# Performance work log

Measured on AMD Instinct MI355X. Metric: run time of the kernel, lower is better.

Reference implementation:

```python
import jax, jax.numpy as jnp
import numpy as np

VOCAB = 50000
WORD_DIM = 300
HIDDEN = 300
REL = 3
B = 512        # batch of (premise, hypothesis) tree pairs
LEAVES = 256   # leaves per complete binary tree (depth 8)


def setup_inputs() -> dict:
    key = jax.random.key(0)
    ks = jax.random.split(key, 6)
    sc = lambda k, shape, s: jax.random.normal(k, shape, dtype=jnp.float32) * s
    return {
        "word_ids": jax.random.randint(ks[0], (B, 2, LEAVES), 0, VOCAB),
        "embedding": sc(ks[1], (VOCAB, WORD_DIM), 0.1),
        "W_leaf": sc(ks[2], (HIDDEN, WORD_DIM), 0.05),   # word2hidden (no bias)
        "W_h": sc(ks[3], (HIDDEN, 2 * HIDDEN), 0.05),    # hidden2hidden
        "b_h": jnp.zeros((HIDDEN,), jnp.float32),
        "W_cls": sc(ks[4], (REL, 2 * HIDDEN), 0.05),
        "b_cls": jnp.zeros((REL,), jnp.float32),
    }


def _encode_trees(word_ids, embedding, W_leaf, W_h, b_h):
    # word_ids: [B, 2, L] leaf token ids of complete binary trees.
    # Leaf: h = word2hidden(embedding(id))  (no bias, no activation)
    h = embedding[word_ids] @ W_leaf.T                     # [B, 2, L, H]
    # Postorder combine, level-synchronous: parent = hidden2hidden(cat(l, r))
    n = h.shape[2]
    while n > 1:
        left = h[:, :, 0::2, :]
        right = h[:, :, 1::2, :]
        h = jnp.concatenate([left, right], axis=-1) @ W_h.T + b_h
        n //= 2
    return h[:, :, 0, :]                                   # [B, 2, H] roots


def reference(word_ids, embedding, W_leaf, W_h, b_h, W_cls, b_cls):
    roots = _encode_trees(word_ids, embedding, W_leaf, W_h, b_h)  # [B, 2, H]
    feat = jax.nn.sigmoid(roots.reshape(roots.shape[0], -1))      # cat(p, h) -> [B, 2H]
    logits = feat @ W_cls.T + b_cls                               # [B, REL]
    return jax.nn.log_softmax(logits, axis=-1)
```

## Files before the change

kernel.cpp:

```cpp
#include <hip/hip_runtime.h>
#include <hip/hip_bf16.h>

typedef __hip_bfloat16 bf16;
typedef __attribute__((ext_vector_type(8))) short short8;
typedef __attribute__((ext_vector_type(4))) float float4v;
typedef __attribute__((ext_vector_type(4))) short short4v;

__device__ __forceinline__ short f2bs(float x) {
    bf16 b = __float2bfloat16(x);
    return *reinterpret_cast<short*>(&b);
}
__device__ __forceinline__ float bs2f(short s) {
    bf16 b = *reinterpret_cast<bf16*>(&s);
    return __bfloat162float(b);
}

#define GLL16(g, l) __builtin_amdgcn_global_load_lds(                      \
    (const __attribute__((address_space(1))) void*)(g),                    \
    (__attribute__((address_space(3))) void*)(l), 16, 0, 0)


__global__ __launch_bounds__(256) void conv_emb(
    const float* __restrict__ src, short* __restrict__ dst)
{
    const int idx = blockIdx.x * 256 + threadIdx.x;
    if (idx >= 50176 * 80) return;
    const int row = idx / 80;
    const int k4  = (idx - row * 80) * 4;
    short4v v = (short4v)0;
    if (row < 50000 && k4 < 300) {
        const float4v f = *reinterpret_cast<const float4v*>(
            src + (long)row * 300 + k4);
#pragma unroll
        for (int j = 0; j < 4; ++j) v[j] = f2bs(f[j]);
    }
    *(short4v*)&dst[(long)row * 320 + k4] = v;
}

__global__ __launch_bounds__(256) void conv_w(
    const float* __restrict__ W_h, const float* __restrict__ W_leaf,
    const float* __restrict__ b_h, short* __restrict__ Bh,
    short* __restrict__ Bleaf, float* __restrict__ biasp)
{
    const int idx = blockIdx.x * 256 + threadIdx.x;
    if (idx < 204800) {
        const int row = idx / 640, k = idx - row * 640;
        float v = 0.f;
        if (row < 300) {
            if (k < 300)                  v = W_h[row * 600 + k];
            else if (k >= 320 && k < 620) v = W_h[row * 600 + k - 20];
        }
        Bh[idx] = f2bs(v);
    } else if (idx < 307200) {
        const int i = idx - 204800;
        const int row = i / 320, k = i - row * 320;
        Bleaf[i] = (row < 300 && k < 300) ? f2bs(W_leaf[row * 300 + k])
                                          : (short)0;
    } else if (idx < 307520) {
        const int i = idx - 307200;
        biasp[i] = (i < 300) ? b_h[i] : 0.f;
    }
}

template <int KE, int GMODE, bool BIAS>
__global__ __launch_bounds__(256, 2) void mfma_gemm(
    const short* __restrict__ Xsrc, const int* __restrict__ wid,
    const short* __restrict__ emb, const short* __restrict__ Wp,
    const float* __restrict__ biasp, short* __restrict__ out)
{
    static_assert(GMODE != 2 || KE == 640, "pair-gather requires KE=640");
    __shared__ __align__(16) short As[2][128 * 32];
    __shared__ __align__(16) short Bs[2][320 * 32];

    const int tid  = threadIdx.x;
    const int lane = tid & 63;
    const int w    = tid >> 6;
    const int wm   = w >> 1, wn = w & 1;
    const long m0  = (long)blockIdx.x * 128;

    const int s_q   = lane & 3;
    const int r_off = lane >> 2;

    const char* gL[2];
    const char* gR[2];
#pragma unroll
    for (int j = 0; j < 2; ++j) {
        const int r = (w * 2 + j) * 16 + r_off;
        const int q = s_q ^ ((r >> 1) & 3);
        if (GMODE == 2) {
            const long node = m0 + r;
            gL[j] = (const char*)emb + (long)wid[2 * node]     * 640 + q * 16;
            gR[j] = (const char*)emb + (long)wid[2 * node + 1] * 640 + q * 16;
        } else {
            gL[j] = (const char*)Xsrc + (m0 + r) * (long)(KE * 2) + q * 16;
            gR[j] = gL[j];
        }
    }
    const char* gB[5];
#pragma unroll
    for (int j = 0; j < 5; ++j) {
        const int r = (w * 5 + j) * 16 + r_off;
        const int q = s_q ^ ((r >> 1) & 3);
        gB[j] = (const char*)Wp + r * (long)(KE * 2) + q * 16;
    }

    int oA[4];
#pragma unroll
    for (int t = 0; t < 4; ++t) {
        const int row = wm * 64 + t * 16 + (lane & 15);
        const int s   = (lane >> 4) ^ ((row >> 1) & 3);
        oA[t] = row * 32 + s * 8;
    }
    int oB[10];
#pragma unroll
    for (int u = 0; u < 10; ++u) {
        const int n = wn * 160 + u * 16 + (lane & 15);
        const int s = (lane >> 4) ^ ((n >> 1) & 3);
        oB[u] = n * 32 + s * 8;
    }

    auto stage = [&](int buf, int kc) {
        char* baseA = (char*)&As[buf][0];
        char* baseB = (char*)&Bs[buf][0];
        if (GMODE == 2) {
            const bool lft = (kc < 10);
            const int off = (lft ? kc : kc - 10) * 64;
            GLL16((lft ? gL[0] : gR[0]) + off, baseA + (w * 2 + 0) * 1024);
            GLL16((lft ? gL[1] : gR[1]) + off, baseA + (w * 2 + 1) * 1024);
        } else {
            const int off = kc * 64;
            GLL16(gL[0] + off, baseA + (w * 2 + 0) * 1024);
            GLL16(gL[1] + off, baseA + (w * 2 + 1) * 1024);
        }
        const int offb = kc * 64;
#pragma unroll
        for (int j = 0; j < 5; ++j)
            GLL16(gB[j] + offb, baseB + (w * 5 + j) * 1024);
    };

    float4v acc[4][10];
#pragma unroll
    for (int t = 0; t < 4; ++t)
#pragma unroll
        for (int u = 0; u < 10; ++u) acc[t][u] = (float4v)0.f;

    const int NCH = KE / 32;
    stage(0, 0);
    for (int kc = 0; kc < NCH; ++kc) {
        const int cur = kc & 1;
        if (kc + 1 < NCH) {
            stage(cur ^ 1, kc + 1);
            asm volatile("s_waitcnt vmcnt(7)" ::: "memory");
        } else {
            asm volatile("s_waitcnt vmcnt(0)" ::: "memory");
        }
        __builtin_amdgcn_s_barrier();
        __builtin_amdgcn_sched_barrier(0);

        const short* bA = &As[cur][0];
        const short* bB = &Bs[cur][0];
        short8 a[4], b[10];
#pragma unroll
        for (int t = 0; t < 4; ++t) a[t] = *(const short8*)(bA + oA[t]);
#pragma unroll
        for (int u = 0; u < 10; ++u) b[u] = *(const short8*)(bB + oB[u]);
#pragma unroll
        for (int u = 0; u < 10; ++u)
#pragma unroll
            for (int t = 0; t < 4; ++t)
                acc[t][u] = __builtin_amdgcn_mfma_f32_16x16x32_bf16(
                    a[t], b[u], acc[t][u], 0, 0, 0);
        __builtin_amdgcn_s_barrier();
    }

#pragma unroll
    for (int u = 0; u < 10; ++u) {
        const int c = wn * 160 + u * 16 + (lane & 15);
        const float bv = BIAS ? biasp[c] : 0.f;
#pragma unroll
        for (int t = 0; t < 4; ++t) {
            const long mb = m0 + wm * 64 + t * 16 + (lane >> 4) * 4;
#pragma unroll
            for (int r4 = 0; r4 < 4; ++r4)
                out[(mb + r4) * 320 + c] = f2bs(acc[t][u][r4] + bv);
        }
    }
}

template<int MA, bool STREAM, bool TOROOTS>
__device__ __forceinline__ void tree_level(
    const int w, const int lane,
    const short* Ain, short* Aout, short* Bs, short* Astage,
    const char* gA, const char* gB0, const char* gB1, const char* gB2,
    const char* gB3, const char* gB4, const float* __restrict__ biasp)
{
    constexpr int MT  = (MA + 15) / 16;
    constexpr int TPW = MT * 5;
    const int lrow = lane & 15;
    const int hi   = lane >> 4;

    float4v acc[TPW];
#pragma unroll
    for (int t = 0; t < TPW; ++t) acc[t] = (float4v)0.f;

    for (int kc = 0; kc < 20; ++kc) {
        GLL16(gB0 + kc * 64, (char*)Bs + (w * 5 + 0) * 1024);
        GLL16(gB1 + kc * 64, (char*)Bs + (w * 5 + 1) * 1024);
        GLL16(gB2 + kc * 64, (char*)Bs + (w * 5 + 2) * 1024);
        GLL16(gB3 + kc * 64, (char*)Bs + (w * 5 + 3) * 1024);
        GLL16(gB4 + kc * 64, (char*)Bs + (w * 5 + 4) * 1024);
        if (STREAM)
            GLL16(gA + (kc >= 10 ? 640 : 0) + (kc % 10) * 64,
                  (char*)Astage + w * 1024);
        asm volatile("s_waitcnt vmcnt(0)" ::: "memory");
        __builtin_amdgcn_s_barrier();
        __builtin_amdgcn_sched_barrier(0);

#pragma unroll
        for (int t = 0; t < TPW; ++t) {
            const int g  = w + t * 4;
            const int mt = g / 20, nt = g % 20;
            int row = mt * 16 + lrow;
            if (MA < 16) row = (lrow < MA) ? lrow : 0;
            const int sa = hi ^ ((row >> 1) & 3);
            const short* pa = STREAM
                ? (Astage + row * 32 + sa * 8)
                : (Ain + kc * (MA * 32) + row * 32 + sa * 8);
            const int n  = nt * 16 + lrow;
            const int sb = hi ^ ((n >> 1) & 3);
            const short8 a = *(const short8*)pa;
            const short8 b = *(const short8*)(Bs + n * 32 + sb * 8);
            acc[t] = __builtin_amdgcn_mfma_f32_16x16x32_bf16(
                a, b, acc[t], 0, 0, 0);
        }
        __builtin_amdgcn_s_barrier();
    }

#pragma unroll
    for (int t = 0; t < TPW; ++t) {
        const int g  = w + t * 4;
        const int mt = g / 20, nt = g % 20;
        const int c  = nt * 16 + lrow;
        const float bv = biasp[c];
#pragma unroll
        for (int r4 = 0; r4 < 4; ++r4) {
            const int mb = mt * 16 + hi * 4 + r4;
            if (mb < MA) {
                const short v = f2bs(acc[t][r4] + bv);
                if (TOROOTS) {
                    Aout[mb * 320 + c] = v;
                } else {
                    constexpr int MN = MA / 2;
                    const int p  = (mb & 1) * 10 + (c >> 5);
                    const int m2 = mb >> 1;
                    const int q  = (c >> 3) & 3;
                    Aout[p * (MN * 32) + m2 * 32 +
                         (q ^ ((m2 >> 1) & 3)) * 8 + (c & 7)] = v;
                }
            }
        }
    }
    __syncthreads();
}

__global__ __launch_bounds__(256, 2) void subtree(
    const short* __restrict__ L2in, const short* __restrict__ Wp,
    const float* __restrict__ biasp, const float* __restrict__ W_cls,
    const float* __restrict__ b_cls, float* __restrict__ outp)
{
    __shared__ __align__(16) short Bs[320 * 32];
    __shared__ __align__(16) short AX[20 * 32 * 32];
    __shared__ __align__(16) short AY[10240];

    const int tid  = threadIdx.x;
    const int lane = tid & 63;
    const int w    = tid >> 6;
    const int s_q   = lane & 3;
    const int r_off = lane >> 2;
    const long base = (long)blockIdx.x * 128;

    const char* gB[5];
#pragma unroll
    for (int j = 0; j < 5; ++j) {
        const int r = (w * 5 + j) * 16 + r_off;
        const int q = s_q ^ ((r >> 1) & 3);
        gB[j] = (const char*)Wp + r * 1280L + q * 16;
    }
    const int rS = w * 16 + r_off;
    const int qS = s_q ^ ((rS >> 1) & 3);
    const char* gA3 = (const char*)L2in + (base + 2 * rS) * 640 + qS * 16;

    tree_level<64, true,  false>(w, lane, nullptr, AX, Bs, AY, gA3,
                                 gB[0], gB[1], gB[2], gB[3], gB[4], biasp);
    tree_level<32, false, false>(w, lane, AX, AY, Bs, nullptr, nullptr,
                                 gB[0], gB[1], gB[2], gB[3], gB[4], biasp);
    tree_level<16, false, false>(w, lane, AY, AX, Bs, nullptr, nullptr,
                                 gB[0], gB[1], gB[2], gB[3], gB[4], biasp);
    tree_level<8,  false, false>(w, lane, AX, AY, Bs, nullptr, nullptr,
                                 gB[0], gB[1], gB[2], gB[3], gB[4], biasp);
    tree_level<4,  false, false>(w, lane, AY, AX, Bs, nullptr, nullptr,
                                 gB[0], gB[1], gB[2], gB[3], gB[4], biasp);
    tree_level<2,  false, true >(w, lane, AX, AY, Bs, nullptr, nullptr,
                                 gB[0], gB[1], gB[2], gB[3], gB[4], biasp);

    if (w == 0) {
        float a0 = 0.f, a1 = 0.f, a2 = 0.f;
#pragma unroll
        for (int i = 0; i < 10; ++i) {
            const int k = lane + 64 * i;
            if (k < 600) {
                const int col = (k < 300) ? k : (320 + k - 300);
                const float f = 1.f / (1.f + __expf(-bs2f(AY[col])));
                a0 += f * W_cls[k];
                a1 += f * W_cls[600 + k];
                a2 += f * W_cls[1200 + k];
            }
        }
#pragma unroll
        for (int off = 32; off > 0; off >>= 1) {
            a0 += __shfl_down(a0, off);
            a1 += __shfl_down(a1, off);
            a2 += __shfl_down(a2, off);
        }
        if (lane == 0) {
            const int b = blockIdx.x;
            const float l0 = a0 + b_cls[0];
            const float l1 = a1 + b_cls[1];
            const float l2 = a2 + b_cls[2];
            const float m  = fmaxf(l0, fmaxf(l1, l2));
            const float s  = __expf(l0 - m) + __expf(l1 - m) + __expf(l2 - m);
            const float ls = m + __logf(s);
            outp[b * 3 + 0] = l0 - ls;
            outp[b * 3 + 1] = l1 - ls;
            outp[b * 3 + 2] = l2 - ls;
        }
    }
}

extern "C" void kernel_launch(void* const* d_in, const int* in_sizes, int n_in,
                              void* d_out, int out_size, void* d_ws, size_t ws_size,
                              hipStream_t stream)
{
    const int*   wid    = (const int*)d_in[0];
    const float* emb    = (const float*)d_in[1];
    const float* W_leaf = (const float*)d_in[2];
    const float* W_h    = (const float*)d_in[3];
    const float* b_h    = (const float*)d_in[4];
    const float* W_cls  = (const float*)d_in[5];
    const float* b_cls  = (const float*)d_in[6];
    float* outp = (float*)d_out;

    (void)in_sizes; (void)n_in; (void)out_size; (void)ws_size;

    char* ws = (char*)d_ws;
    short* bufA   = (short*)(ws);
    short* bufB   = (short*)(ws + 83886080);
    short* emb_bf = (short*)(ws + 83886080);
    short* Hv     = (short*)(ws + 125829120);
    short* Bleaf  = (short*)(ws + 157941760);
    short* Bh     = (short*)(ws + 158146560);
    float* biasp  = (float*)(ws + 158556160);

    conv_emb<<<(50176 * 80) / 256, 256, 0, stream>>>(emb, emb_bf);
    conv_w  <<<(307520 + 255) / 256, 256, 0, stream>>>(
        W_h, W_leaf, b_h, Bh, Bleaf, biasp);

    mfma_gemm<320, 0, false><<<50176 / 128, 256, 0, stream>>>(
        emb_bf, nullptr, nullptr, Bleaf, biasp, Hv);

    mfma_gemm<640, 2, true><<<131072 / 128, 256, 0, stream>>>(
        nullptr, wid, Hv, Bh, biasp, bufA);

    mfma_gemm<640, 0, true><<<65536 / 128, 256, 0, stream>>>(
        bufA, nullptr, nullptr, Bh, biasp, bufB);

    subtree<<<512, 256, 0, stream>>>(bufB, Bh, biasp, W_cls, b_cls, outp);
}
```

Baseline: 343.8 us.

## Process two trees per subtree block sharing weight tiles, merge conversion kernels

The subtree kernel now runs 512 threads handling two tree pairs per block. Waves 0-3 load the shared W_h tile into LDS while waves 4-7 stream both trees' level inputs, so each weight chunk is fetched once per two trees and the blocks are halved. The two fp32-to-bf16 conversion kernels are merged into one launch to save launch overhead. The costs are more LDS per block, occupancy capped at one 512-thread block, and load work concentrated on fewer waves.

```diff
diff --git a/kernel.cpp b/kernel.cpp
--- a/kernel.cpp
+++ b/kernel.cpp
@@ -19,45 +19,42 @@
     (const __attribute__((address_space(1))) void*)(g),                    \
     (__attribute__((address_space(3))) void*)(l), 16, 0, 0)
 
-
-__global__ __launch_bounds__(256) void conv_emb(
-    const float* __restrict__ src, short* __restrict__ dst)
+__global__ __launch_bounds__(256) void conv_all(
+    const float* __restrict__ emb, const float* __restrict__ W_h,
+    const float* __restrict__ W_leaf, const float* __restrict__ b_h,
+    short* __restrict__ emb_bf, short* __restrict__ Bh,
+    short* __restrict__ Bleaf, float* __restrict__ biasp)
 {
     const int idx = blockIdx.x * 256 + threadIdx.x;
-    if (idx >= 50176 * 80) return;
-    const int row = idx / 80;
-    const int k4  = (idx - row * 80) * 4;
-    short4v v = (short4v)0;
-    if (row < 50000 && k4 < 300) {
-        const float4v f = *reinterpret_cast<const float4v*>(
-            src + (long)row * 300 + k4);
-#pragma unroll
-        for (int j = 0; j < 4; ++j) v[j] = f2bs(f[j]);
-    }
-    *(short4v*)&dst[(long)row * 320 + k4] = v;
-}
-
-__global__ __launch_bounds__(256) void conv_w(
-    const float* __restrict__ W_h, const float* __restrict__ W_leaf,
-    const float* __restrict__ b_h, short* __restrict__ Bh,
-    short* __restrict__ Bleaf, float* __restrict__ biasp)
-{
-    const int idx = blockIdx.x * 256 + threadIdx.x;
-    if (idx < 204800) {
-        const int row = idx / 640, k = idx - row * 640;
+    if (idx < 4014080) {
+        const int row = idx / 80;
+        const int k4  = (idx - row * 80) * 4;
+        short4v v = (short4v)0;
+        if (row < 50000 && k4 < 300) {
+            const float4v f = *reinterpret_cast<const float4v*>(
+                emb + (long)row * 300 + k4);
+#pragma unroll
+            for (int j = 0; j < 4; ++j) v[j] = f2bs(f[j]);
+        }
+        *(short4v*)&emb_bf[(long)row * 320 + k4] = v;
+        return;
+    }
+    const int j = idx - 4014080;
+    if (j < 204800) {
+        const int row = j / 640, k = j - row * 640;
         float v = 0.f;
         if (row < 300) {
             if (k < 300)                  v = W_h[row * 600 + k];
             else if (k >= 320 && k < 620) v = W_h[row * 600 + k - 20];
         }
-        Bh[idx] = f2bs(v);
-    } else if (idx < 307200) {
-        const int i = idx - 204800;
+        Bh[j] = f2bs(v);
+    } else if (j < 307200) {
+        const int i = j - 204800;
         const int row = i / 320, k = i - row * 320;
         Bleaf[i] = (row < 300 && k < 300) ? f2bs(W_leaf[row * 300 + k])
                                           : (short)0;
-    } else if (idx < 307520) {
-        const int i = idx - 307200;
+    } else if (j < 307520) {
+        const int i = j - 307200;
         biasp[i] = (i < 300) ? b_h[i] : 0.f;
     }
 }
@@ -189,9 +186,11 @@
 
 template<int MA, bool STREAM, bool TOROOTS>
 __device__ __forceinline__ void tree_level(
-    const int w, const int lane,
-    const short* Ain, short* Aout, short* Bs, short* Astage,
-    const char* gA, const char* gB0, const char* gB1, const char* gB2,
+    const int w, const int wl, const int lane,
+    const short* Ain, short* Aout, short* Bs,
+    const short* myAst, short* Ast0, short* Ast1,
+    const char* gA0, const char* gA1,
+    const char* gB0, const char* gB1, const char* gB2,
     const char* gB3, const char* gB4, const float* __restrict__ biasp)
 {
     constexpr int MT  = (MA + 15) / 16;
@@ -204,27 +203,30 @@
     for (int t = 0; t < TPW; ++t) acc[t] = (float4v)0.f;
 
     for (int kc = 0; kc < 20; ++kc) {
-        GLL16(gB0 + kc * 64, (char*)Bs + (w * 5 + 0) * 1024);
-        GLL16(gB1 + kc * 64, (char*)Bs + (w * 5 + 1) * 1024);
-        GLL16(gB2 + kc * 64, (char*)Bs + (w * 5 + 2) * 1024);
-        GLL16(gB3 + kc * 64, (char*)Bs + (w * 5 + 3) * 1024);
-        GLL16(gB4 + kc * 64, (char*)Bs + (w * 5 + 4) * 1024);
-        if (STREAM)
-            GLL16(gA + (kc >= 10 ? 640 : 0) + (kc % 10) * 64,
-                  (char*)Astage + w * 1024);
+        if (w < 4) {
+            GLL16(gB0 + kc * 64, (char*)Bs + (w * 5 + 0) * 1024);
+            GLL16(gB1 + kc * 64, (char*)Bs + (w * 5 + 1) * 1024);
+            GLL16(gB2 + kc * 64, (char*)Bs + (w * 5 + 2) * 1024);
+            GLL16(gB3 + kc * 64, (char*)Bs + (w * 5 + 3) * 1024);
+            GLL16(gB4 + kc * 64, (char*)Bs + (w * 5 + 4) * 1024);
+        } else if (STREAM) {
+            const int off = (kc >= 10 ? 640 : 0) + (kc % 10) * 64;
+            GLL16(gA0 + off, (char*)Ast0 + (w - 4) * 1024);
+            GLL16(gA1 + off, (char*)Ast1 + (w - 4) * 1024);
+        }
         asm volatile("s_waitcnt vmcnt(0)" ::: "memory");
         __builtin_amdgcn_s_barrier();
         __builtin_amdgcn_sched_barrier(0);
 
 #pragma unroll
         for (int t = 0; t < TPW; ++t) {
-            const int g  = w + t * 4;
+            const int g  = wl + t * 4;
             const int mt = g / 20, nt = g % 20;
             int row = mt * 16 + lrow;
             if (MA < 16) row = (lrow < MA) ? lrow : 0;
             const int sa = hi ^ ((row >> 1) & 3);
             const short* pa = STREAM
-                ? (Astage + row * 32 + sa * 8)
+                ? (myAst + row * 32 + sa * 8)
                 : (Ain + kc * (MA * 32) + row * 32 + sa * 8);
             const int n  = nt * 16 + lrow;
             const int sb = hi ^ ((n >> 1) & 3);
@@ -238,7 +240,7 @@
 
 #pragma unroll
     for (int t = 0; t < TPW; ++t) {
-        const int g  = w + t * 4;
+        const int g  = wl + t * 4;
         const int mt = g / 20, nt = g % 20;
         const int c  = nt * 16 + lrow;
         const float bv = biasp[c];
@@ -263,54 +265,69 @@
     __syncthreads();
 }
 
-__global__ __launch_bounds__(256, 2) void subtree(
+__global__ __launch_bounds__(512, 1) void subtree(
     const short* __restrict__ L2in, const short* __restrict__ Wp,
     const float* __restrict__ biasp, const float* __restrict__ W_cls,
     const float* __restrict__ b_cls, float* __restrict__ outp)
 {
     __shared__ __align__(16) short Bs[320 * 32];
-    __shared__ __align__(16) short AX[20 * 32 * 32];
-    __shared__ __align__(16) short AY[10240];
+    __shared__ __align__(16) short AXs[2][20 * 32 * 32];
+    __shared__ __align__(16) short AYs[2][10240];
+    __shared__ __align__(16) short Ast[2][2048];
 
     const int tid  = threadIdx.x;
     const int lane = tid & 63;
     const int w    = tid >> 6;
+    const int wl   = w & 3;
+    const int grp  = w >> 2;
     const int s_q   = lane & 3;
     const int r_off = lane >> 2;
-    const long base = (long)blockIdx.x * 128;
 
     const char* gB[5];
 #pragma unroll
     for (int j = 0; j < 5; ++j) {
-        const int r = (w * 5 + j) * 16 + r_off;
+        const int r = (wl * 5 + j) * 16 + r_off;
         const int q = s_q ^ ((r >> 1) & 3);
         gB[j] = (const char*)Wp + r * 1280L + q * 16;
     }
-    const int rS = w * 16 + r_off;
+    const int wa = (w >= 4) ? (w - 4) : 0;
+    const int rS = wa * 16 + r_off;
     const int qS = s_q ^ ((rS >> 1) & 3);
-    const char* gA3 = (const char*)L2in + (base + 2 * rS) * 640 + qS * 16;
-
-    tree_level<64, true,  false>(w, lane, nullptr, AX, Bs, AY, gA3,
-                                 gB[0], gB[1], gB[2], gB[3], gB[4], biasp);
-    tree_level<32, false, false>(w, lane, AX, AY, Bs, nullptr, nullptr,
-                                 gB[0], gB[1], gB[2], gB[3], gB[4], biasp);
-    tree_level<16, false, false>(w, lane, AY, AX, Bs, nullptr, nullptr,
-                                 gB[0], gB[1], gB[2], gB[3], gB[4], biasp);
-    tree_level<8,  false, false>(w, lane, AX, AY, Bs, nullptr, nullptr,
-                                 gB[0], gB[1], gB[2], gB[3], gB[4], biasp);
-    tree_level<4,  false, false>(w, lane, AY, AX, Bs, nullptr, nullptr,
-                                 gB[0], gB[1], gB[2], gB[3], gB[4], biasp);
-    tree_level<2,  false, true >(w, lane, AX, AY, Bs, nullptr, nullptr,
-                                 gB[0], gB[1], gB[2], gB[3], gB[4], biasp);
-
-    if (w == 0) {
+    const long base0 = (long)(2 * blockIdx.x) * 128;
+    const char* gA0 = (const char*)L2in + (base0 + 2 * rS) * 640 + qS * 16;
+    const char* gA1 = (const char*)L2in + (base0 + 128 + 2 * rS) * 640 + qS * 16;
+
+    short* AXm = AXs[grp];
+    short* AYm = AYs[grp];
+
+    tree_level<64, true,  false>(w, wl, lane, nullptr, AXm, Bs,
+                                 Ast[grp], Ast[0], Ast[1], gA0, gA1,
+                                 gB[0], gB[1], gB[2], gB[3], gB[4], biasp);
+    tree_level<32, false, false>(w, wl, lane, AXm, AYm, Bs,
+                                 nullptr, nullptr, nullptr, nullptr, nullptr,
+                                 gB[0], gB[1], gB[2], gB[3], gB[4], biasp);
+    tree_level<16, false, false>(w, wl, lane, AYm, AXm, Bs,
+                                 nullptr, nullptr, nullptr, nullptr, nullptr,
+                                 gB[0], gB[1], gB[2], gB[3], gB[4], biasp);
+    tree_level<8,  false, false>(w, wl, lane, AXm, AYm, Bs,
+                                 nullptr, nullptr, nullptr, nullptr, nullptr,
+                                 gB[0], gB[1], gB[2], gB[3], gB[4], biasp);
+    tree_level<4,  false, false>(w, wl, lane, AYm, AXm, Bs,
+                                 nullptr, nullptr, nullptr, nullptr, nullptr,
+                                 gB[0], gB[1], gB[2], gB[3], gB[4], biasp);
+    tree_level<2,  false, true >(w, wl, lane, AXm, AYm, Bs,
+                                 nullptr, nullptr, nullptr, nullptr, nullptr,
+                                 gB[0], gB[1], gB[2], gB[3], gB[4], biasp);
+
+    if (wl == 0) {
+        const short* rowp = AYs[grp];
         float a0 = 0.f, a1 = 0.f, a2 = 0.f;
 #pragma unroll
         for (int i = 0; i < 10; ++i) {
             const int k = lane + 64 * i;
             if (k < 600) {
                 const int col = (k < 300) ? k : (320 + k - 300);
-                const float f = 1.f / (1.f + __expf(-bs2f(AY[col])));
+                const float f = 1.f / (1.f + __expf(-bs2f(rowp[col])));
                 a0 += f * W_cls[k];
                 a1 += f * W_cls[600 + k];
                 a2 += f * W_cls[1200 + k];
@@ -323,7 +340,7 @@
             a2 += __shfl_down(a2, off);
         }
         if (lane == 0) {
-            const int b = blockIdx.x;
+            const int b = blockIdx.x * 2 + grp;
             const float l0 = a0 + b_cls[0];
             const float l1 = a1 + b_cls[1];
             const float l2 = a2 + b_cls[2];
@@ -361,9 +378,8 @@
     short* Bh     = (short*)(ws + 158146560);
     float* biasp  = (float*)(ws + 158556160);
 
-    conv_emb<<<(50176 * 80) / 256, 256, 0, stream>>>(emb, emb_bf);
-    conv_w  <<<(307520 + 255) / 256, 256, 0, stream>>>(
-        W_h, W_leaf, b_h, Bh, Bleaf, biasp);
+    conv_all<<<(4321600 + 255) / 256, 256, 0, stream>>>(
+        emb, W_h, W_leaf, b_h, emb_bf, Bh, Bleaf, biasp);
 
     mfma_gemm<320, 0, false><<<50176 / 128, 256, 0, stream>>>(
         emb_bf, nullptr, nullptr, Bleaf, biasp, Hv);
@@ -374,5 +390,5 @@
     mfma_gemm<640, 0, true><<<65536 / 128, 256, 0, stream>>>(
         bufA, nullptr, nullptr, Bh, biasp, bufB);
 
-    subtree<<<512, 256, 0, stream>>>(bufB, Bh, biasp, W_cls, b_cls, outp);
-}
+    subtree<<<256, 512, 0, stream>>>(bufB, Bh, biasp, W_cls, b_cls, outp);
+}
```

Result: faster. 304.0 us (-11.6%).
